# Kernel tuning notes

Measured on AMD Instinct MI355X. Metric: run time of the kernel, lower is better.

Reference implementation:

```python
import jax, jax.numpy as jnp
import numpy as np

EPS = 1e-5
SCALES = jnp.array([7.0, 7.0, 4.0], dtype=jnp.float32)  # (W, H, T) per source buffer
OUT_T, OUT_H, OUT_W = 3, 5, 5


def _roi_align3d(feat, start, end):
    """feat: [C,T,H,W]; start/end: [3] = (x, y, t). One sample per bin (bin center),
    trilinear interpolation, out-of-bounds -> 0 (standard ROIAlign convention)."""
    C, T, H, W = feat.shape
    dt = feat.dtype

    def centers(s, e, n):
        b = (e - s) / n
        return s + (jnp.arange(n, dtype=dt) + 0.5) * b

    xc = centers(start[0], end[0], OUT_W)  # [Wo]
    yc = centers(start[1], end[1], OUT_H)  # [Ho]
    tc = centers(start[2], end[2], OUT_T)  # [To]

    def prep(c, size):
        valid = ((c >= -1.0) & (c <= size)).astype(dt)
        c = jnp.clip(c, 0.0, size - 1)
        lo = jnp.floor(c).astype(jnp.int32)
        hi = jnp.minimum(lo + 1, size - 1)
        f = c - lo.astype(dt)
        return (lo, hi), ((1.0 - f) * valid, f * valid)

    ti, tw = prep(tc, T)
    yi, yw = prep(yc, H)
    xi, xw = prep(xc, W)

    out = jnp.zeros((C, OUT_T, OUT_H, OUT_W), dtype=dt)
    for a in range(2):
        for b in range(2):
            for c in range(2):
                g = feat[:, ti[a][:, None, None], yi[b][None, :, None], xi[c][None, None, :]]
                w = tw[a][:, None, None] * yw[b][None, :, None] * xw[c][None, None, :]
                out = out + g * w
    return out


def setup_inputs() -> dict:
    key = jax.random.key(0)
    k0, k1, k2 = jax.random.split(key, 3)
    B, C, T, H, W = 128, 1024, 4, 7, 7
    R = 256
    x = jax.random.normal(k0, (B, C, T, H, W), jnp.float32)
    w1 = jax.random.normal(k1, (R, C), jnp.float32) / np.sqrt(C).astype(np.float32)
    w2 = jax.random.normal(k2, (6, R), jnp.float32) / np.sqrt(R).astype(np.float32)
    return dict(
        x=x, w1=w1,
        g1=jnp.ones((R,), jnp.float32), b1=jnp.zeros((R,), jnp.float32),
        m1=jnp.zeros((R,), jnp.float32), v1=jnp.ones((R,), jnp.float32),
        w2=w2,
        g2=jnp.ones((6,), jnp.float32), b2=jnp.zeros((6,), jnp.float32),
        m2=jnp.zeros((6,), jnp.float32), v2=jnp.ones((6,), jnp.float32),
    )


def reference(x, w1, g1, b1, m1, v1, w2, g2, b2, m2, v2):
    # roi head: conv1x1x1 -> BN(eval) -> HSwish -> global avgpool -> conv1x1x1 -> BN(eval)
    h = jnp.einsum('bcthw,rc->brthw', x, w1)
    s1 = (g1 / jnp.sqrt(v1 + EPS))
    h = (h - m1[None, :, None, None, None]) * s1[None, :, None, None, None] + b1[None, :, None, None, None]
    h = h * jnp.clip(h + 3.0, 0.0, 6.0) * (1.0 / 6.0)  # HSwish
    h = h.mean(axis=(2, 3, 4))                          # AvgPool3d over full (T,H,W) -> [B,R]
    logits = h @ w2.T
    logits = (logits - m2) * (g2 / jnp.sqrt(v2 + EPS)) + b2  # [B,6]
    raw = jax.nn.sigmoid(logits)
    roi_start = 0.5 * raw[:, :3] * SCALES              # (x1,y1,t1)
    roi_end = (1.0 - 0.5 * raw[:, 3:]) * SCALES        # (x2,y2,t2)
    return jax.vmap(_roi_align3d)(x, roi_start, roi_end)  # [B,C,3,5,5]
```

## Files before the change

### kernel.cpp

```cpp
#include <hip/hip_runtime.h>

typedef __bf16 bf16x8 __attribute__((ext_vector_type(8)));
typedef float f32x4 __attribute__((ext_vector_type(4)));

#define EPS_F 1e-5f

__device__ __forceinline__ unsigned short f2bf(float f) {
    unsigned int u;
    __builtin_memcpy(&u, &f, 4);
    unsigned int r = (u + 0x7fffu + ((u >> 16) & 1u)) >> 16;
    return (unsigned short)r;
}

__global__ __launch_bounds__(512) void k_gemm_pool(
    const float* __restrict__ x,
    const float* __restrict__ w1,
    const float* __restrict__ g1,
    const float* __restrict__ b1,
    const float* __restrict__ m1,
    const float* __restrict__ v1,
    float* __restrict__ pooled)
{
    constexpr int LDK = 40;
    __shared__ unsigned short Alds[224 * LDK];
    __shared__ unsigned short Blds[64 * LDK];
    __shared__ float pool_lds[2][64];

    const int b   = blockIdx.x;
    const int r0  = blockIdx.y * 64;
    const int tid = threadIdx.x;
    const int wave = tid >> 6, lane = tid & 63;
    const int wm = wave >> 2, wn = wave & 3;
    const int q  = lane >> 4, ln = lane & 15;

    f32x4 acc[7];
#pragma unroll
    for (int i = 0; i < 7; i++) acc[i] = (f32x4){0.f, 0.f, 0.f, 0.f};

    const int c4  = tid & 7;
    const int p4  = tid >> 3;
    const bool a_act = (p4 < 56);
    const bool a_val = (p4 < 49);
    const float* xb = x + (size_t)b * 1024 * 196 + p4 * 4;

    const int rB = tid >> 3, k16 = tid & 7;

    for (int kc = 0; kc < 1024; kc += 32) {
        __syncthreads();
        {
            const float4 f = *(const float4*)(w1 + (size_t)(r0 + rB) * 1024 + kc + k16 * 4);
            ushort4 o;
            o.x = f2bf(f.x); o.y = f2bf(f.y); o.z = f2bf(f.z); o.w = f2bf(f.w);
            *(ushort4*)&Blds[rB * LDK + k16 * 4] = o;
        }
        if (a_act) {
            float fv[4][4];
            if (a_val) {
#pragma unroll
                for (int i = 0; i < 4; i++) {
                    const float4 f = *(const float4*)(xb + (size_t)(kc + c4 * 4 + i) * 196);
                    fv[i][0] = f.x; fv[i][1] = f.y; fv[i][2] = f.z; fv[i][3] = f.w;
                }
            } else {
#pragma unroll
                for (int i = 0; i < 4; i++)
#pragma unroll
                    for (int j = 0; j < 4; j++) fv[i][j] = 0.f;
            }
#pragma unroll
            for (int j = 0; j < 4; j++) {
                ushort4 o;
                o.x = f2bf(fv[0][j]);
                o.y = f2bf(fv[1][j]);
                o.z = f2bf(fv[2][j]);
                o.w = f2bf(fv[3][j]);
                *(ushort4*)&Alds[(p4 * 4 + j) * LDK + c4 * 4] = o;
            }
        }
        __syncthreads();
        const bf16x8 bfr = *(const bf16x8*)&Blds[(wn * 16 + ln) * LDK + q * 8];
#pragma unroll
        for (int mi = 0; mi < 7; mi++) {
            const int mt = wm * 7 + mi;
            const bf16x8 af = *(const bf16x8*)&Alds[(mt * 16 + ln) * LDK + q * 8];
            acc[mi] = __builtin_amdgcn_mfma_f32_16x16x32_bf16(af, bfr, acc[mi], 0, 0, 0);
        }
    }

    float psum = 0.f;
    {
        const int r = r0 + wn * 16 + ln;
        const float s1 = g1[r] * rsqrtf(v1[r] + EPS_F);
        const float mu = m1[r];
        const float be = b1[r];
#pragma unroll
        for (int mi = 0; mi < 7; mi++) {
            const int mt = wm * 7 + mi;
#pragma unroll
            for (int i = 0; i < 4; i++) {
                const int m = mt * 16 + q * 4 + i;
                if (m < 196) {
                    float v = acc[mi][i];
                    v = (v - mu) * s1 + be;
                    const float g = fminf(fmaxf(v + 3.f, 0.f), 6.f);
                    psum += v * g * (1.f / 6.f);
                }
            }
        }
    }
    psum += __shfl_xor(psum, 16, 64);
    psum += __shfl_xor(psum, 32, 64);
    if (lane < 16) pool_lds[wm][wn * 16 + lane] = psum;
    __syncthreads();
    if (tid < 64)
        pooled[b * 256 + r0 + tid] =
            (pool_lds[0][tid] + pool_lds[1][tid]) * (1.f / 196.f);
}

__global__ __launch_bounds__(64) void k_logits(
    const float* __restrict__ pooled,
    const float* __restrict__ w2,
    const float* __restrict__ g2,
    const float* __restrict__ b2,
    const float* __restrict__ m2,
    const float* __restrict__ v2,
    float* __restrict__ roi)
{
    const int b = blockIdx.x, t = threadIdx.x;
    const float4 p4 = ((const float4*)(pooled + b * 256))[t];
    float part[6];
#pragma unroll
    for (int j = 0; j < 6; j++) {
        const float4 w = *(const float4*)(w2 + j * 256 + t * 4);
        part[j] = p4.x * w.x + p4.y * w.y + p4.z * w.z + p4.w * w.w;
    }
#pragma unroll
    for (int j = 0; j < 6; j++)
#pragma unroll
        for (int off = 32; off >= 1; off >>= 1)
            part[j] += __shfl_xor(part[j], off, 64);
    if (t == 0) {
        const float SC[3] = {7.f, 7.f, 4.f};
        float raw[6];
#pragma unroll
        for (int j = 0; j < 6; j++) {
            float l = part[j];
            const float s = g2[j] * rsqrtf(v2[j] + EPS_F);
            l = (l - m2[j]) * s + b2[j];
            raw[j] = 1.f / (1.f + expf(-l));
        }
#pragma unroll
        for (int d = 0; d < 3; d++) {
            roi[b * 6 + d]     = 0.5f * raw[d] * SC[d];
            roi[b * 6 + 3 + d] = (1.f - 0.5f * raw[3 + d]) * SC[d];
        }
    }
}

__device__ __forceinline__ void prep1(float s, float e, int n, int size, int i,
                                      int& lo, int& hi, float& w0, float& w1)
{
    const float bsz = (e - s) / (float)n;
    float c = s + ((float)i + 0.5f) * bsz;
    const float valid = (c >= -1.f && c <= (float)size) ? 1.f : 0.f;
    c = fminf(fmaxf(c, 0.f), (float)(size - 1));
    lo = (int)floorf(c);
    hi = min(lo + 1, size - 1);
    const float f = c - (float)lo;
    w0 = (1.f - f) * valid;
    w1 = f * valid;
}

__global__ __launch_bounds__(256) void k_roi(
    const float* __restrict__ x,
    const float* __restrict__ roi,
    float* __restrict__ out)
{
    __shared__ float xs[32 * 200];
    __shared__ int   soff[8][80];
    __shared__ float swt[8][80];

    const int b = blockIdx.x, c0 = blockIdx.y * 32;
    const int tid = threadIdx.x;

    const float* xb = x + ((size_t)b * 1024 + c0) * 196;
#pragma unroll
    for (int k = 0; k < 7; k++) {
        const int i4 = tid + k * 256;
        if (i4 < 1568) {
            const int c = i4 / 49, pq = i4 % 49;
            const float4 v = *(const float4*)(xb + c * 196 + pq * 4);
            *(float4*)&xs[c * 200 + pq * 4] = v;
        }
    }
    if (tid < 75) {
        const int po = tid;
        const int to = po / 25, rem = po % 25, yo = rem / 5, xo = rem % 5;
        const float sx = roi[b * 6 + 0], ex = roi[b * 6 + 3];
        const float sy = roi[b * 6 + 1], ey = roi[b * 6 + 4];
        const float st = roi[b * 6 + 2], et = roi[b * 6 + 5];
        int tl, th, yl, yh, xl, xh;
        float tw0, tw1, yw0, yw1, xw0, xw1;
        prep1(st, et, 3, 4, to, tl, th, tw0, tw1);
        prep1(sy, ey, 5, 7, yo, yl, yh, yw0, yw1);
        prep1(sx, ex, 5, 7, xo, xl, xh, xw0, xw1);
#pragma unroll
        for (int s = 0; s < 8; s++) {
            const int   ti = (s & 4) ? th : tl;
            const int   yi = (s & 2) ? yh : yl;
            const int   xi = (s & 1) ? xh : xl;
            const float w = ((s & 4) ? tw1 : tw0) *
                            ((s & 2) ? yw1 : yw0) *
                            ((s & 1) ? xw1 : xw0);
            soff[s][po] = ti * 49 + yi * 7 + xi;
            swt[s][po]  = w;
        }
    }
    __syncthreads();

    const size_t obase = ((size_t)b * 1024 + c0) * 75;
#pragma unroll
    for (int k = 0; k < 10; k++) {
        const int e = tid + k * 256;
        if (e < 2400) {
            const int c = e / 75, po = e % 75;
            const float* row = &xs[c * 200];
            float v = 0.f;
#pragma unroll
            for (int s = 0; s < 8; s++)
                v += swt[s][po] * row[soff[s][po]];
            out[obase + e] = v;
        }
    }
}

extern "C" void kernel_launch(void* const* d_in, const int* in_sizes, int n_in,
                              void* d_out, int out_size, void* d_ws, size_t ws_size,
                              hipStream_t stream)
{
    const float* x  = (const float*)d_in[0];
    const float* w1 = (const float*)d_in[1];
    const float* g1 = (const float*)d_in[2];
    const float* b1 = (const float*)d_in[3];
    const float* m1 = (const float*)d_in[4];
    const float* v1 = (const float*)d_in[5];
    const float* w2 = (const float*)d_in[6];
    const float* g2 = (const float*)d_in[7];
    const float* b2 = (const float*)d_in[8];
    const float* m2 = (const float*)d_in[9];
    const float* v2 = (const float*)d_in[10];

    float* pooled = (float*)d_ws;
    float* roi    = pooled + 128 * 256;
    float* out    = (float*)d_out;

    k_gemm_pool<<<dim3(128, 4), 512, 0, stream>>>(x, w1, g1, b1, m1, v1, pooled);
    k_logits<<<128, 64, 0, stream>>>(pooled, w2, g2, b2, m2, v2, roi);
    k_roi<<<dim3(128, 32), 256, 0, stream>>>(x, roi, out);
}
```

Before: 240.5 us.

## Split GEMM-pool spatial dimension across two blocks and use native bf16 conversion

The GEMM+pool kernel's 196 spatial rows are split into two halves along a new grid z dimension, doubling the block count from 512 to 1024 and shrinking per-block LDS and accumulators. Each half writes partial pooled sums that the logits kernel adds together. The manual round-to-nearest-even bf16 conversion is replaced with native __bf16 casts, and launch bounds now request higher occupancy. The cost is that each block loads w1 tiles redundantly, and the uneven split leaves one wave row idle for part of the work.

```diff
diff --git a/kernel.cpp b/kernel.cpp
--- a/kernel.cpp
+++ b/kernel.cpp
@@ -1,47 +1,44 @@
 #include <hip/hip_runtime.h>
 
 typedef __bf16 bf16x8 __attribute__((ext_vector_type(8)));
+typedef __bf16 bf16x4 __attribute__((ext_vector_type(4)));
 typedef float f32x4 __attribute__((ext_vector_type(4)));
 
 #define EPS_F 1e-5f
 
-__device__ __forceinline__ unsigned short f2bf(float f) {
-    unsigned int u;
-    __builtin_memcpy(&u, &f, 4);
-    unsigned int r = (u + 0x7fffu + ((u >> 16) & 1u)) >> 16;
-    return (unsigned short)r;
-}
-
-__global__ __launch_bounds__(512) void k_gemm_pool(
+__global__ __launch_bounds__(512, 8) void k_gemm_pool(
     const float* __restrict__ x,
     const float* __restrict__ w1,
     const float* __restrict__ g1,
     const float* __restrict__ b1,
     const float* __restrict__ m1,
     const float* __restrict__ v1,
-    float* __restrict__ pooled)
+    float* __restrict__ pooled_part)
 {
     constexpr int LDK = 40;
-    __shared__ unsigned short Alds[224 * LDK];
-    __shared__ unsigned short Blds[64 * LDK];
+    __shared__ __bf16 Alds[112 * LDK];
+    __shared__ __bf16 Blds[64 * LDK];
     __shared__ float pool_lds[2][64];
 
     const int b   = blockIdx.x;
     const int r0  = blockIdx.y * 64;
+    const int mc  = blockIdx.z;
     const int tid = threadIdx.x;
     const int wave = tid >> 6, lane = tid & 63;
     const int wm = wave >> 2, wn = wave & 3;
     const int q  = lane >> 4, ln = lane & 15;
-
-    f32x4 acc[7];
-#pragma unroll
-    for (int i = 0; i < 7; i++) acc[i] = (f32x4){0.f, 0.f, 0.f, 0.f};
+    const int nm = (wm == 0) ? 4 : 3;
+
+    f32x4 acc[4];
+#pragma unroll
+    for (int i = 0; i < 4; i++) acc[i] = (f32x4){0.f, 0.f, 0.f, 0.f};
 
     const int c4  = tid & 7;
     const int p4  = tid >> 3;
-    const bool a_act = (p4 < 56);
-    const bool a_val = (p4 < 49);
-    const float* xb = x + (size_t)b * 1024 * 196 + p4 * 4;
+    const bool a_act = (p4 < 28);
+    const int  pg    = mc * 28 + p4;
+    const bool a_val = a_act && (pg < 49);
+    const float* xb = x + (size_t)b * 1024 * 196 + pg * 4;
 
     const int rB = tid >> 3, k16 = tid & 7;
 
@@ -49,9 +46,8 @@
         __syncthreads();
         {
             const float4 f = *(const float4*)(w1 + (size_t)(r0 + rB) * 1024 + kc + k16 * 4);
-            ushort4 o;
-            o.x = f2bf(f.x); o.y = f2bf(f.y); o.z = f2bf(f.z); o.w = f2bf(f.w);
-            *(ushort4*)&Blds[rB * LDK + k16 * 4] = o;
+            bf16x4 o = {(__bf16)f.x, (__bf16)f.y, (__bf16)f.z, (__bf16)f.w};
+            *(bf16x4*)&Blds[rB * LDK + k16 * 4] = o;
         }
         if (a_act) {
             float fv[4][4];
@@ -69,21 +65,20 @@
             }
 #pragma unroll
             for (int j = 0; j < 4; j++) {
-                ushort4 o;
-                o.x = f2bf(fv[0][j]);
-                o.y = f2bf(fv[1][j]);
-                o.z = f2bf(fv[2][j]);
-                o.w = f2bf(fv[3][j]);
-                *(ushort4*)&Alds[(p4 * 4 + j) * LDK + c4 * 4] = o;
+                bf16x4 o = {(__bf16)fv[0][j], (__bf16)fv[1][j],
+                            (__bf16)fv[2][j], (__bf16)fv[3][j]};
+                *(bf16x4*)&Alds[(p4 * 4 + j) * LDK + c4 * 4] = o;
             }
         }
         __syncthreads();
         const bf16x8 bfr = *(const bf16x8*)&Blds[(wn * 16 + ln) * LDK + q * 8];
 #pragma unroll
-        for (int mi = 0; mi < 7; mi++) {
-            const int mt = wm * 7 + mi;
-            const bf16x8 af = *(const bf16x8*)&Alds[(mt * 16 + ln) * LDK + q * 8];
-            acc[mi] = __builtin_amdgcn_mfma_f32_16x16x32_bf16(af, bfr, acc[mi], 0, 0, 0);
+        for (int mi = 0; mi < 4; mi++) {
+            if (mi < nm) {
+                const int mt = wm * 4 + mi;
+                const bf16x8 af = *(const bf16x8*)&Alds[(mt * 16 + ln) * LDK + q * 8];
+                acc[mi] = __builtin_amdgcn_mfma_f32_16x16x32_bf16(af, bfr, acc[mi], 0, 0, 0);
+            }
         }
     }
 
@@ -94,16 +89,18 @@
         const float mu = m1[r];
         const float be = b1[r];
 #pragma unroll
-        for (int mi = 0; mi < 7; mi++) {
-            const int mt = wm * 7 + mi;
-#pragma unroll
-            for (int i = 0; i < 4; i++) {
-                const int m = mt * 16 + q * 4 + i;
-                if (m < 196) {
-                    float v = acc[mi][i];
-                    v = (v - mu) * s1 + be;
-                    const float g = fminf(fmaxf(v + 3.f, 0.f), 6.f);
-                    psum += v * g * (1.f / 6.f);
+        for (int mi = 0; mi < 4; mi++) {
+            if (mi < nm) {
+                const int mt = wm * 4 + mi;
+#pragma unroll
+                for (int i = 0; i < 4; i++) {
+                    const int m = mc * 112 + mt * 16 + q * 4 + i;
+                    if (m < 196) {
+                        float v = acc[mi][i];
+                        v = (v - mu) * s1 + be;
+                        const float g = fminf(fmaxf(v + 3.f, 0.f), 6.f);
+                        psum += v * g * (1.f / 6.f);
+                    }
                 }
             }
         }
@@ -113,12 +110,12 @@
     if (lane < 16) pool_lds[wm][wn * 16 + lane] = psum;
     __syncthreads();
     if (tid < 64)
-        pooled[b * 256 + r0 + tid] =
+        pooled_part[(size_t)mc * (128 * 256) + b * 256 + r0 + tid] =
             (pool_lds[0][tid] + pool_lds[1][tid]) * (1.f / 196.f);
 }
 
 __global__ __launch_bounds__(64) void k_logits(
-    const float* __restrict__ pooled,
+    const float* __restrict__ pooled_part,
     const float* __restrict__ w2,
     const float* __restrict__ g2,
     const float* __restrict__ b2,
@@ -127,7 +124,11 @@
     float* __restrict__ roi)
 {
     const int b = blockIdx.x, t = threadIdx.x;
-    const float4 p4 = ((const float4*)(pooled + b * 256))[t];
+    const float4 pa = ((const float4*)(pooled_part + b * 256))[t];
+    const float4 pb = ((const float4*)(pooled_part + 128 * 256 + b * 256))[t];
+    float4 p4;
+    p4.x = pa.x + pb.x; p4.y = pa.y + pb.y;
+    p4.z = pa.z + pb.z; p4.w = pa.w + pb.w;
     float part[6];
 #pragma unroll
     for (int j = 0; j < 6; j++) {
@@ -250,11 +251,11 @@
     const float* m2 = (const float*)d_in[9];
     const float* v2 = (const float*)d_in[10];
 
-    float* pooled = (float*)d_ws;
-    float* roi    = pooled + 128 * 256;
-    float* out    = (float*)d_out;
-
-    k_gemm_pool<<<dim3(128, 4), 512, 0, stream>>>(x, w1, g1, b1, m1, v1, pooled);
-    k_logits<<<128, 64, 0, stream>>>(pooled, w2, g2, b2, m2, v2, roi);
+    float* pooled_part = (float*)d_ws;
+    float* roi         = pooled_part + 2 * 128 * 256;
+    float* out         = (float*)d_out;
+
+    k_gemm_pool<<<dim3(128, 4, 2), 512, 0, stream>>>(x, w1, g1, b1, m1, v1, pooled_part);
+    k_logits<<<128, 64, 0, stream>>>(pooled_part, w2, g2, b2, m2, v2, roi);
     k_roi<<<dim3(128, 32), 256, 0, stream>>>(x, roi, out);
 }
```

After: 244.8 us. Within noise of the previous version (+1.8%).
